# Kernel tuning notes

Measured on AMD Instinct MI355X. Metric: run time of the kernel, lower is better.

The kernel has to match this reference:

```python
import jax, jax.numpy as jnp
import numpy as np
import math

B, T, D, H = 4, 1024, 1024, 16
DK = D // H
EPS = 1e-12  # F.normalize eps

def setup_inputs() -> dict:
    key = jax.random.key(0)
    ks = jax.random.split(key, 6)
    xav = math.sqrt(6.0 / (D + D))  # xavier_uniform bound for square Linear
    x = jax.random.normal(ks[0], (B, T, D), dtype=jnp.float32)
    Wq = jax.random.uniform(ks[1], (D, D), jnp.float32, -xav, xav)
    Wk = jax.random.uniform(ks[2], (D, D), jnp.float32, -xav, xav)
    Wv = jax.random.uniform(ks[3], (D, D), jnp.float32, -xav, xav)
    Wo = jax.random.uniform(ks[4], (D, D), jnp.float32, -xav, xav)
    logit_g = math.log(0.9 / 0.1)
    logit_l = math.log(0.1 / 0.9)
    W_gamma = jnp.zeros((H,), jnp.float32)
    b_gamma = jnp.full((H,), logit_g, jnp.float32)
    W_lambda = jnp.zeros((H,), jnp.float32)
    b_lambda = jnp.full((H,), logit_l, jnp.float32)
    return {"x": x, "Wq": Wq, "Wk": Wk, "Wv": Wv, "Wo": Wo,
            "W_gamma": W_gamma, "b_gamma": b_gamma,
            "W_lambda": W_lambda, "b_lambda": b_lambda}

def reference(x, Wq, Wk, Wv, Wo, W_gamma, b_gamma, W_lambda, b_lambda):
    b, t, d = x.shape
    # projections (torch Linear: x @ W.T), split heads -> [T, B, H, dk] for scan
    def proj(W):
        return jnp.einsum('btd,ed->bte', x, W).reshape(b, t, H, DK).transpose(1, 0, 2, 3)
    q = proj(Wq)
    k = proj(Wk)
    v = proj(Wv)
    # L2-normalize k along dk (F.normalize semantics)
    k = k / jnp.maximum(jnp.linalg.norm(k, axis=-1, keepdims=True), EPS)
    k_bar = k.mean(axis=-1)  # [T, B, H]
    gamma = jax.nn.sigmoid(W_gamma * k_bar + b_gamma)
    lam = jax.nn.sigmoid(W_lambda * k_bar + b_lambda)
    rho = (1.0 - lam) * gamma  # [T, B, H]

    S0 = jnp.zeros((b, H, DK, DK), x.dtype)

    def step(S, inp):
        q_t, k_t, v_t, rho_t = inp  # [B,H,dk] x3, [B,H]
        r = rho_t[..., None, None]
        S = r * S + (1.0 - r) * jnp.einsum('bhv,bhk->bhvk', v_t, k_t)
        y_t = jnp.einsum('bhv,bhvk->bhk', q_t, S)
        return S, y_t

    _, ys = jax.lax.scan(step, S0, (q, k, v, rho))  # ys: [T, B, H, dk]
    out = ys.transpose(1, 0, 2, 3).reshape(b, t, d)
    return jnp.einsum('btd,ed->bte', out, Wo)
```

## Files before the change

### kernel.cpp

```cpp
#include <hip/hip_runtime.h>
#include <hip/hip_bf16.h>


typedef __bf16 b16x8 __attribute__((ext_vector_type(8)));
typedef float  f32x4 __attribute__((ext_vector_type(4)));
typedef unsigned short u16x8 __attribute__((ext_vector_type(8)));
using bf16_t = __hip_bfloat16;

#define AS1C(p) ((const __attribute__((address_space(1))) void*)(p))
#define AS3(p)  ((__attribute__((address_space(3))) void*)(p))

__device__ __forceinline__ void g2l16(const void* g, void* l) {
  __builtin_amdgcn_global_load_lds(AS1C(g), AS3(l), 16, 0, 0);
}
__device__ __forceinline__ void g2l4(const void* g, void* l) {
  __builtin_amdgcn_global_load_lds(AS1C(g), AS3(l), 4, 0, 0);
}

__device__ __forceinline__ unsigned short f2b(float x) {
  unsigned u = __float_as_uint(x);
  return (unsigned short)((u + 0x7FFFu + ((u >> 16) & 1u)) >> 16);
}
__device__ __forceinline__ float b2f(unsigned short b) {
  return __uint_as_float(((unsigned)b) << 16);
}

__device__ __forceinline__ int wire_flag(const unsigned* __restrict__ x, int tid) {
  unsigned u = x[tid & 63];
  int e = (int)((u >> 23) & 0xFF);
  unsigned long long m = __ballot(e >= 95 && e <= 135);
  return (__popcll(m) >= 32) ? 1 : 0;
}

__global__ __launch_bounds__(256)
void convert_all(const void* __restrict__ x,
                 const void* __restrict__ w0, const void* __restrict__ w1,
                 const void* __restrict__ w2, const void* __restrict__ w3,
                 unsigned short* __restrict__ xb,
                 unsigned short* __restrict__ wb0, unsigned short* __restrict__ wb1,
                 unsigned short* __restrict__ wb2, unsigned short* __restrict__ wb3)
{
  const int fm = wire_flag((const unsigned*)x, threadIdx.x);
  const long i8 = ((long)blockIdx.x * 256 + threadIdx.x) * 8;
  const void* src; unsigned short* dst; long off;
  if (i8 < 4194304) { src = x; dst = xb; off = i8; }
  else {
    long j = i8 - 4194304;
    int w = (int)(j >> 20); off = j & 1048575;
    src = (w == 0) ? w0 : (w == 1) ? w1 : (w == 2) ? w2 : w3;
    dst = (w == 0) ? wb0 : (w == 1) ? wb1 : (w == 2) ? wb2 : wb3;
  }
  if (fm) {
    const float4 a = *(const float4*)((const float*)src + off);
    const float4 b = *(const float4*)((const float*)src + off + 4);
    u16x8 o;
    o[0] = f2b(a.x); o[1] = f2b(a.y); o[2] = f2b(a.z); o[3] = f2b(a.w);
    o[4] = f2b(b.x); o[5] = f2b(b.y); o[6] = f2b(b.z); o[7] = f2b(b.w);
    *(u16x8*)(dst + off) = o;
  } else {
    *(int4*)(dst + off) = *(const int4*)((const unsigned short*)src + off);
  }
}

__global__ __launch_bounds__(256)
void gemm_qkv(const unsigned* __restrict__ xraw,
              const bf16_t* __restrict__ A,
              const bf16_t* __restrict__ B0, const bf16_t* __restrict__ B1,
              const bf16_t* __restrict__ B2,
              unsigned short* __restrict__ C0, unsigned short* __restrict__ C1,
              unsigned short* __restrict__ C2,
              const void* __restrict__ Wg, const void* __restrict__ bg,
              const void* __restrict__ Wl, const void* __restrict__ bl,
              float* __restrict__ rho)
{
  constexpr int K = 1024, N = 1024;
  const int flat = blockIdx.x;
  const int xcd = flat & 7, sl = flat >> 3;
  const int z = sl >> 5, t5 = sl & 31;
  const int bx = ((xcd & 1) << 2) | (t5 & 3);
  const int by = ((xcd >> 1) << 3) | (t5 >> 2);
  const bf16_t* B = (z == 0) ? B0 : (z == 1) ? B1 : B2;
  unsigned short* C = (z == 0) ? C0 : (z == 1) ? C1 : C2;
  __shared__ __align__(16) unsigned short As[128 * 32];
  __shared__ __align__(16) unsigned short Bs[128 * 32];
  const int tid  = threadIdx.x;
  const int lane = tid & 63;
  const int wave = tid >> 6;
  const int wm = wave >> 1, wn = wave & 1;
  const int quad = lane >> 4, tm = lane & 15;
  const long row0 = (long)by * 128;
  const long col0 = (long)bx * 128;

  f32x4 acc[4][4];
#pragma unroll
  for (int i = 0; i < 4; ++i)
#pragma unroll
    for (int j = 0; j < 4; ++j) acc[i][j] = (f32x4){0.f, 0.f, 0.f, 0.f};

  const int sr = tid >> 2;
  const int scc = tid & 3;
  const int qg = (scc - (sr >> 1)) & 3;
  const bf16_t* ap = A + (row0 + sr) * (long)K + qg * 8;
  const bf16_t* bp = B + (col0 + sr) * (long)K + qg * 8;
  unsigned short* la = As + tid * 8;
  unsigned short* lb = Bs + tid * 8;
  const int cc = (quad + ((tm >> 1) & 3)) & 3;

  for (int kt = 0; kt < K; kt += 32) {
    __syncthreads();
    g2l16(ap + kt,           la);
    g2l16(ap + 64l * K + kt, la + 2048);
    g2l16(bp + kt,           lb);
    g2l16(bp + 64l * K + kt, lb + 2048);
    __syncthreads();

    b16x8 af[4], bfr[4];
#pragma unroll
    for (int i = 0; i < 4; ++i)
      af[i] = *(const b16x8*)&As[(wm * 64 + i * 16 + tm) * 32 + cc * 8];
#pragma unroll
    for (int j = 0; j < 4; ++j)
      bfr[j] = *(const b16x8*)&Bs[(wn * 64 + j * 16 + tm) * 32 + cc * 8];
#pragma unroll
    for (int i = 0; i < 4; ++i)
#pragma unroll
      for (int j = 0; j < 4; ++j)
        acc[i][j] = __builtin_amdgcn_mfma_f32_16x16x32_bf16(af[i], bfr[j], acc[i][j], 0, 0, 0);
  }

  if (z != 1) {
#pragma unroll
    for (int i = 0; i < 4; ++i)
#pragma unroll
      for (int j = 0; j < 4; ++j)
#pragma unroll
        for (int r = 0; r < 4; ++r) {
          long row = row0 + wm * 64 + i * 16 + quad * 4 + r;
          long col = col0 + wn * 64 + j * 16 + tm;
          C[row * N + col] = f2b(acc[i][j][r]);
        }
  } else {
    const int fm = wire_flag(xraw, tid);
    const int h = bx * 2 + wn;
    float wgv, bgv, wlv, blv;
    if (fm) {
      wgv = ((const float*)Wg)[h]; bgv = ((const float*)bg)[h];
      wlv = ((const float*)Wl)[h]; blv = ((const float*)bl)[h];
    } else {
      wgv = b2f(((const unsigned short*)Wg)[h]); bgv = b2f(((const unsigned short*)bg)[h]);
      wlv = b2f(((const unsigned short*)Wl)[h]); blv = b2f(((const unsigned short*)bl)[h]);
    }
#pragma unroll
    for (int i = 0; i < 4; ++i)
#pragma unroll
      for (int r = 0; r < 4; ++r) {
        float ss = 0.f, sv = 0.f;
#pragma unroll
        for (int j = 0; j < 4; ++j) {
          const float v = acc[i][j][r];
          ss += v * v; sv += v;
        }
#pragma unroll
        for (int m = 1; m < 16; m <<= 1) {
          ss += __shfl_xor(ss, m);
          sv += __shfl_xor(sv, m);
        }
        const float inv = 1.f / fmaxf(sqrtf(ss), 1e-12f);
        const long row = row0 + wm * 64 + i * 16 + quad * 4 + r;
#pragma unroll
        for (int j = 0; j < 4; ++j)
          C[row * N + col0 + wn * 64 + j * 16 + tm] = f2b(acc[i][j][r] * inv);
        if (tm == 0) {
          const float kbar = sv * inv * (1.f / 64.f);
          const float gm = 1.f / (1.f + expf(-(wgv * kbar + bgv)));
          const float lm = 1.f / (1.f + expf(-(wlv * kbar + blv)));
          const int b = (int)(row >> 10), t = (int)(row & 1023);
          rho[(size_t)(b * 16 + h) * 1024 + t] = (1.f - lm) * gm;
        }
      }
  }
}

__global__ __launch_bounds__(256)
void gemm_out64(const unsigned* __restrict__ xraw,
                const bf16_t* __restrict__ A, const bf16_t* __restrict__ B,
                void* __restrict__ C)
{
  constexpr int K = 1024, N = 1024;
  const int flat = blockIdx.x;
  const int xcd = flat & 7, sl = flat >> 3;
  const int bx = sl & 15;
  const int by = (xcd << 3) | (sl >> 4);
  __shared__ __align__(16) unsigned short As[64 * 64];
  __shared__ __align__(16) unsigned short Bs[64 * 64];
  const int tid  = threadIdx.x;
  const int lane = tid & 63;
  const int wave = tid >> 6;
  const int quad = lane >> 4, tm = lane & 15;
  const long row0 = (long)by * 64;
  const long col0 = (long)bx * 64;

  f32x4 acc[4];
#pragma unroll
  for (int i = 0; i < 4; ++i) acc[i] = (f32x4){0.f, 0.f, 0.f, 0.f};

  const int sr = tid >> 2;
  const int scc = tid & 3;
  const int qg = (scc - (sr >> 1)) & 3;
  const bf16_t* ap = A + (row0 + sr) * (long)K + qg * 8;
  const bf16_t* bp = B + (col0 + sr) * (long)K + qg * 8;
  unsigned short* la = As + tid * 8;
  unsigned short* lb = Bs + tid * 8;
  const int cc = (quad + ((tm >> 1) & 3)) & 3;

  for (int kt = 0; kt < K; kt += 64) {
    __syncthreads();
    g2l16(ap + kt,      la);
    g2l16(ap + kt + 32, la + 2048);
    g2l16(bp + kt,      lb);
    g2l16(bp + kt + 32, lb + 2048);
    __syncthreads();

    b16x8 bf0 = *(const b16x8*)&Bs[(wave * 16 + tm) * 32 + cc * 8];
    b16x8 bf1 = *(const b16x8*)&Bs[2048 + (wave * 16 + tm) * 32 + cc * 8];
#pragma unroll
    for (int i = 0; i < 4; ++i) {
      b16x8 a0 = *(const b16x8*)&As[(i * 16 + tm) * 32 + cc * 8];
      b16x8 a1 = *(const b16x8*)&As[2048 + (i * 16 + tm) * 32 + cc * 8];
      acc[i] = __builtin_amdgcn_mfma_f32_16x16x32_bf16(a0, bf0, acc[i], 0, 0, 0);
      acc[i] = __builtin_amdgcn_mfma_f32_16x16x32_bf16(a1, bf1, acc[i], 0, 0, 0);
    }
  }

  const int fm = wire_flag(xraw, tid);
#pragma unroll
  for (int i = 0; i < 4; ++i)
#pragma unroll
    for (int r = 0; r < 4; ++r) {
      const long row = row0 + i * 16 + quad * 4 + r;
      const long col = col0 + wave * 16 + tm;
      const float v = acc[i][r];
      if (fm) ((float*)C)[row * N + col] = v;
      else    ((unsigned short*)C)[row * N + col] = f2b(v);
    }
}

__device__ __forceinline__ void stage_chunk_x(const unsigned short* G, int n0c, int h,
                                              unsigned short* lds, int tid) {
#pragma unroll
  for (int sh = 0; sh < 2; ++sh) {
    const int idx = sh * 256 + tid;
    const int row = idx >> 3, c2 = idx & 7;
    const int gc = c2 ^ (row & 7);
    g2l16(G + (size_t)(n0c + row) * 1024 + h * 64 + gc * 8, lds + idx * 8);
  }
}
__device__ __forceinline__ void stage_blk_x(const unsigned short* G,
                                            unsigned short* lds, int tid) {
#pragma unroll
  for (int sh = 0; sh < 2; ++sh) {
    const int idx = sh * 256 + tid;
    const int row = idx >> 3, c2 = idx & 7;
    const int gc = c2 ^ (row & 7);
    g2l16(G + row * 64 + gc * 8, lds + idx * 8);
  }
}
__device__ __forceinline__ b16x8 rdx(const unsigned short* lds, int row, int k0) {
  return *(const b16x8*)&lds[row * 64 + (((k0 >> 3) ^ (row & 7)) << 3)];
}
__device__ __forceinline__ float rdx1(const unsigned short* lds, int row, int col) {
  return b2f(lds[row * 64 + (((col >> 3) ^ (row & 7)) << 3) + (col & 7)]);
}

__device__ __forceinline__ void transpose_x(const unsigned short* src,
                                            unsigned short* dst,
                                            const float* sc, int tid) {
  const int kc = tid & 63;
  const int s4 = (tid >> 6) * 16;
  u16x8 o0, o1;
#pragma unroll
  for (int i = 0; i < 16; ++i) {
    const int s = s4 + i;
    float v = rdx1(src, s, kc);
    if (sc) v *= sc[s];
    const unsigned short b = f2b(v);
    if (i < 8) o0[i] = b; else o1[i - 8] = b;
  }
  *(u16x8*)&dst[kc * 72 + s4]     = o0;
  *(u16x8*)&dst[kc * 72 + s4 + 8] = o1;
}

__device__ __forceinline__ void rho_scan(const float* rho_s, float* aw, float* cw,
                                         float* sc, int tid) {
  if (tid < 64) {
    const float r = rho_s[tid];
    float p = r;
#pragma unroll
    for (int d = 1; d < 64; d <<= 1) {
      float o = __shfl_up(p, d);
      if (tid >= d) p *= o;
    }
    aw[tid] = p;
    const float c = (1.f - r) / p;
    cw[tid] = c;
    const float Ac = __shfl(p, 63);
    sc[tid] = Ac * c;
  }
}

__global__ __launch_bounds__(256)
void chunk_outer(const unsigned short* __restrict__ Kb, const unsigned short* __restrict__ Vb,
                 const float* __restrict__ rho, unsigned short* __restrict__ Ug,
                 float* __restrict__ A_g)
{
  __shared__ __align__(16) unsigned short ks[4096];
  __shared__ __align__(16) unsigned short vs[4096];
  __shared__ __align__(16) unsigned short kt[64 * 72];
  __shared__ __align__(16) unsigned short vt[64 * 72];
  __shared__ float rho_s[64], aw[64], cw[64], sc[64];
  const int tid = threadIdx.x;
  const int bid = blockIdx.x;
  const int bh = bid >> 4, c = bid & 15;
  const int b = bh >> 4, h = bh & 15;
  const int n0c = b * 1024 + c * 64;
  const int lane = tid & 63, wave = tid >> 6;
  const int quad = lane >> 4, tm = lane & 15;

  stage_chunk_x(Kb, n0c, h, ks, tid);
  stage_chunk_x(Vb, n0c, h, vs, tid);
  if (tid < 64) g2l4(rho + (size_t)bh * 1024 + c * 64 + tid, rho_s + tid);
  __syncthreads();
  rho_scan(rho_s, aw, cw, sc, tid);
  __syncthreads();
  transpose_x(ks, kt, sc, tid);
  transpose_x(vs, vt, nullptr, tid);
  __syncthreads();

  const int mrow = 16 * wave + tm;
  b16x8 a0 = *(const b16x8*)&kt[mrow * 72 + quad * 8];
  b16x8 a1 = *(const b16x8*)&kt[mrow * 72 + 32 + quad * 8];
#pragma unroll
  for (int j4 = 0; j4 < 4; ++j4) {
    const int nrow = 16 * j4 + tm;
    b16x8 b0 = *(const b16x8*)&vt[nrow * 72 + quad * 8];
    b16x8 b1 = *(const b16x8*)&vt[nrow * 72 + 32 + quad * 8];
    f32x4 acc = (f32x4){0.f, 0.f, 0.f, 0.f};
    acc = __builtin_amdgcn_mfma_f32_16x16x32_bf16(a0, b0, acc, 0, 0, 0);
    acc = __builtin_amdgcn_mfma_f32_16x16x32_bf16(a1, b1, acc, 0, 0, 0);
#pragma unroll
    for (int r = 0; r < 4; ++r) {
      const int kc = 16 * wave + quad * 4 + r;
      Ug[(size_t)bid * 4096 + kc * 64 + 16 * j4 + tm] = f2b(acc[r]);
    }
  }
  if (tid == 0) A_g[bid] = aw[63];
}

__global__ __launch_bounds__(256)
void chunk_scan(const unsigned short* __restrict__ Ug, const float* __restrict__ A_g,
                unsigned short* __restrict__ Sp)
{
  const int bh = blockIdx.x >> 4;
  const int e  = (blockIdx.x & 15) * 256 + threadIdx.x;
  const size_t base = (size_t)bh * 16 * 4096 + e;
  float S = 0.f;
#pragma unroll
  for (int c = 0; c < 16; ++c) {
    Sp[base + (size_t)c * 4096] = f2b(S);
    S = A_g[bh * 16 + c] * S + b2f(Ug[base + (size_t)c * 4096]);
  }
}

__global__ __launch_bounds__(256)
void chunk_y(const unsigned short* __restrict__ Qb, const unsigned short* __restrict__ Kb,
             const unsigned short* __restrict__ Vb, const unsigned short* __restrict__ Sp,
             const float* __restrict__ rho, unsigned short* __restrict__ Yb)
{
  __shared__ __align__(16) unsigned short qs[4096];
  __shared__ __align__(16) unsigned short ks[4096];
  __shared__ __align__(16) unsigned short vs[4096];
  __shared__ __align__(16) unsigned short ss[4096];
  __shared__ __align__(16) unsigned short kt[64 * 72];
  __shared__ __align__(16) unsigned short pt[64 * 72];
  __shared__ float rho_s[64], aw[64], cw[64], sc[64];
  const int tid = threadIdx.x;
  const int bid = blockIdx.x;
  const int bh = bid >> 4, c = bid & 15;
  const int b = bh >> 4, h = bh & 15;
  const int n0c = b * 1024 + c * 64;
  const int lane = tid & 63, wave = tid >> 6;
  const int quad = lane >> 4, tm = lane & 15;

  stage_chunk_x(Qb, n0c, h, qs, tid);
  stage_chunk_x(Kb, n0c, h, ks, tid);
  stage_chunk_x(Vb, n0c, h, vs, tid);
  stage_blk_x(Sp + (size_t)bid * 4096, ss, tid);
  if (tid < 64) g2l4(rho + (size_t)bh * 1024 + c * 64 + tid, rho_s + tid);
  __syncthreads();
  rho_scan(rho_s, aw, cw, sc, tid);
  __syncthreads();
  transpose_x(ks, kt, nullptr, tid);

  __bf16* ptb = (__bf16*)pt;
  const int trow = 16 * wave + tm;

  b16x8 af_q[2];
#pragma unroll
  for (int kk = 0; kk < 2; ++kk)
    af_q[kk] = rdx(qs, trow, kk * 32 + quad * 8);
#pragma unroll
  for (int j4 = 0; j4 < 4; ++j4) {
    f32x4 acc = (f32x4){0.f, 0.f, 0.f, 0.f};
#pragma unroll
    for (int kk = 0; kk < 2; ++kk) {
      const b16x8 bf = rdx(vs, 16 * j4 + tm, kk * 32 + quad * 8);
      acc = __builtin_amdgcn_mfma_f32_16x16x32_bf16(af_q[kk], bf, acc, 0, 0, 0);
    }
    const int s = 16 * j4 + tm;
    const float cws = cw[s];
#pragma unroll
    for (int r = 0; r < 4; ++r) {
      const int t = 16 * wave + quad * 4 + r;
      const float w = (s <= t) ? aw[t] * cws : 0.f;
      ptb[t * 72 + s] = (__bf16)(acc[r] * w);
    }
  }

  const float at = aw[trow];
  b16x8 af_qs[2], af_p[2];
#pragma unroll
  for (int kk = 0; kk < 2; ++kk) {
    b16x8 t8;
#pragma unroll
    for (int j = 0; j < 8; ++j) t8[j] = (__bf16)(at * (float)af_q[kk][j]);
    af_qs[kk] = t8;
    af_p[kk] = *(const b16x8*)&pt[trow * 72 + kk * 32 + quad * 8];
  }
  __syncthreads();

#pragma unroll
  for (int j4 = 0; j4 < 4; ++j4) {
    const int kc = 16 * j4 + tm;
    f32x4 acc = (f32x4){0.f, 0.f, 0.f, 0.f};
#pragma unroll
    for (int kk = 0; kk < 2; ++kk) {
      const int kbase = kk * 32 + quad * 8;
      const b16x8 bk = *(const b16x8*)&kt[kc * 72 + kbase];
      const b16x8 bs = rdx(ss, kc, kbase);
      acc = __builtin_amdgcn_mfma_f32_16x16x32_bf16(af_p[kk],  bk, acc, 0, 0, 0);
      acc = __builtin_amdgcn_mfma_f32_16x16x32_bf16(af_qs[kk], bs, acc, 0, 0, 0);
    }
#pragma unroll
    for (int r = 0; r < 4; ++r) {
      const int t = 16 * wave + quad * 4 + r;
      Yb[(size_t)(n0c + t) * 1024 + h * 64 + kc] = f2b(acc[r]);
    }
  }
}

extern "C" void kernel_launch(void* const* d_in, const int* in_sizes, int n_in,
                              void* d_out, int out_size, void* d_ws, size_t ws_size,
                              hipStream_t stream) {
  const void* x  = d_in[0];
  const void* Wq = d_in[1];
  const void* Wk = d_in[2];
  const void* Wv = d_in[3];
  const void* Wo = d_in[4];

  char* ws = (char*)d_ws;
  const size_t MB = 1ull << 20;
  unsigned short* x_b  = (unsigned short*)(ws);
  unsigned short* Wq_b = (unsigned short*)(ws + 8 * MB);
  unsigned short* Wk_b = (unsigned short*)(ws + 10 * MB);
  unsigned short* Wv_b = (unsigned short*)(ws + 12 * MB);
  unsigned short* Wo_b = (unsigned short*)(ws + 14 * MB);
  unsigned short* Qb = (unsigned short*)(ws + 16 * MB);
  unsigned short* Kb = (unsigned short*)(ws + 24 * MB);
  unsigned short* Vb = (unsigned short*)(ws + 32 * MB);
  unsigned short* Yb = (unsigned short*)(ws + 40 * MB);
  unsigned short* Ug = (unsigned short*)(ws + 48 * MB);
  unsigned short* Sp = (unsigned short*)(ws + 64 * MB);
  float*  rh   = (float*)(ws + 72 * MB);
  float*  A_g  = (float*)(ws + 72 * MB + 256 * 1024);

  dim3 blk(256);
  convert_all<<<dim3(4096), blk, 0, stream>>>(x, Wq, Wk, Wv, Wo,
                                              x_b, Wq_b, Wk_b, Wv_b, Wo_b);
  gemm_qkv<<<dim3(768), blk, 0, stream>>>((const unsigned*)x,
      (const bf16_t*)x_b, (const bf16_t*)Wq_b, (const bf16_t*)Wk_b, (const bf16_t*)Wv_b,
      Qb, Kb, Vb, d_in[5], d_in[6], d_in[7], d_in[8], rh);
  chunk_outer<<<dim3(1024), blk, 0, stream>>>(Kb, Vb, rh, Ug, A_g);
  chunk_scan<<<dim3(1024), blk, 0, stream>>>(Ug, A_g, Sp);
  chunk_y<<<dim3(1024), blk, 0, stream>>>(Qb, Kb, Vb, Sp, rh, Yb);
  gemm_out64<<<dim3(1024), blk, 0, stream>>>((const unsigned*)x,
      (const bf16_t*)Yb, (const bf16_t*)Wo_b, d_out);
}
```

Before: 168.9 us.

## Fuse chunked scan into one sequential per-head kernel and widen GEMM K tile

Replaces the three chunk kernels (outer products, inter-chunk scan, intra-chunk output) with one kernel per batch-head. It walks the 16 chunks sequentially, keeps the running state in registers and LDS, and double-buffers the Q/K/V chunk loads. This removes the global round trips for the per-chunk updates and prefix states, plus two launches. The cost is that the grid shrinks from 1024 to 64 blocks and the chunks are serialized. The QKV GEMM also moves to a 64-wide K tile with XOR-swizzled LDS, which halves the barriers per K step.

```diff
diff --git a/kernel.cpp b/kernel.cpp
--- a/kernel.cpp
+++ b/kernel.cpp
@@ -12,9 +12,6 @@
 
 __device__ __forceinline__ void g2l16(const void* g, void* l) {
   __builtin_amdgcn_global_load_lds(AS1C(g), AS3(l), 16, 0, 0);
-}
-__device__ __forceinline__ void g2l4(const void* g, void* l) {
-  __builtin_amdgcn_global_load_lds(AS1C(g), AS3(l), 4, 0, 0);
 }
 
 __device__ __forceinline__ unsigned short f2b(float x) {
@@ -81,8 +78,8 @@
   const int by = ((xcd >> 1) << 3) | (t5 >> 2);
   const bf16_t* B = (z == 0) ? B0 : (z == 1) ? B1 : B2;
   unsigned short* C = (z == 0) ? C0 : (z == 1) ? C1 : C2;
-  __shared__ __align__(16) unsigned short As[128 * 32];
-  __shared__ __align__(16) unsigned short Bs[128 * 32];
+  __shared__ __align__(16) unsigned short As[128 * 64];
+  __shared__ __align__(16) unsigned short Bs[128 * 64];
   const int tid  = threadIdx.x;
   const int lane = tid & 63;
   const int wave = tid >> 6;
@@ -97,35 +94,39 @@
 #pragma unroll
     for (int j = 0; j < 4; ++j) acc[i][j] = (f32x4){0.f, 0.f, 0.f, 0.f};
 
-  const int sr = tid >> 2;
-  const int scc = tid & 3;
-  const int qg = (scc - (sr >> 1)) & 3;
-  const bf16_t* ap = A + (row0 + sr) * (long)K + qg * 8;
-  const bf16_t* bp = B + (col0 + sr) * (long)K + qg * 8;
+  const int sr = tid >> 3;
+  const int c2 = tid & 7;
+  const int gc = c2 ^ (sr & 7);
+  const bf16_t* ap = A + (row0 + sr) * (long)K + gc * 8;
+  const bf16_t* bp = B + (col0 + sr) * (long)K + gc * 8;
   unsigned short* la = As + tid * 8;
   unsigned short* lb = Bs + tid * 8;
-  const int cc = (quad + ((tm >> 1) & 3)) & 3;
-
-  for (int kt = 0; kt < K; kt += 32) {
-    __syncthreads();
-    g2l16(ap + kt,           la);
-    g2l16(ap + 64l * K + kt, la + 2048);
-    g2l16(bp + kt,           lb);
-    g2l16(bp + 64l * K + kt, lb + 2048);
-    __syncthreads();
-
-    b16x8 af[4], bfr[4];
-#pragma unroll
-    for (int i = 0; i < 4; ++i)
-      af[i] = *(const b16x8*)&As[(wm * 64 + i * 16 + tm) * 32 + cc * 8];
-#pragma unroll
-    for (int j = 0; j < 4; ++j)
-      bfr[j] = *(const b16x8*)&Bs[(wn * 64 + j * 16 + tm) * 32 + cc * 8];
-#pragma unroll
-    for (int i = 0; i < 4; ++i)
+
+  for (int kt = 0; kt < K; kt += 64) {
+    __syncthreads();
+#pragma unroll
+    for (int sh = 0; sh < 4; ++sh) {
+      g2l16(ap + (long)sh * 32 * K + kt, la + sh * 2048);
+      g2l16(bp + (long)sh * 32 * K + kt, lb + sh * 2048);
+    }
+    __syncthreads();
+
+#pragma unroll
+    for (int kk = 0; kk < 2; ++kk) {
+      const int pcsel = ((kk * 4 + quad) ^ (tm & 7)) << 3;
+      b16x8 af[4], bfr[4];
+#pragma unroll
+      for (int i = 0; i < 4; ++i)
+        af[i] = *(const b16x8*)&As[(wm * 64 + i * 16 + tm) * 64 + pcsel];
 #pragma unroll
       for (int j = 0; j < 4; ++j)
-        acc[i][j] = __builtin_amdgcn_mfma_f32_16x16x32_bf16(af[i], bfr[j], acc[i][j], 0, 0, 0);
+        bfr[j] = *(const b16x8*)&Bs[(wn * 64 + j * 16 + tm) * 64 + pcsel];
+#pragma unroll
+      for (int i = 0; i < 4; ++i)
+#pragma unroll
+        for (int j = 0; j < 4; ++j)
+          acc[i][j] = __builtin_amdgcn_mfma_f32_16x16x32_bf16(af[i], bfr[j], acc[i][j], 0, 0, 0);
+    }
   }
 
   if (z != 1) {
@@ -255,16 +256,6 @@
     g2l16(G + (size_t)(n0c + row) * 1024 + h * 64 + gc * 8, lds + idx * 8);
   }
 }
-__device__ __forceinline__ void stage_blk_x(const unsigned short* G,
-                                            unsigned short* lds, int tid) {
-#pragma unroll
-  for (int sh = 0; sh < 2; ++sh) {
-    const int idx = sh * 256 + tid;
-    const int row = idx >> 3, c2 = idx & 7;
-    const int gc = c2 ^ (row & 7);
-    g2l16(G + row * 64 + gc * 8, lds + idx * 8);
-  }
-}
 __device__ __forceinline__ b16x8 rdx(const unsigned short* lds, int row, int k0) {
   return *(const b16x8*)&lds[row * 64 + (((k0 >> 3) ^ (row & 7)) << 3)];
 }
@@ -273,188 +264,156 @@
 }
 
 __device__ __forceinline__ void transpose_x(const unsigned short* src,
-                                            unsigned short* dst,
-                                            const float* sc, int tid) {
+                                            unsigned short* dst, int tid) {
   const int kc = tid & 63;
   const int s4 = (tid >> 6) * 16;
   u16x8 o0, o1;
 #pragma unroll
   for (int i = 0; i < 16; ++i) {
-    const int s = s4 + i;
-    float v = rdx1(src, s, kc);
-    if (sc) v *= sc[s];
-    const unsigned short b = f2b(v);
+    const unsigned short b = f2b(rdx1(src, s4 + i, kc));
     if (i < 8) o0[i] = b; else o1[i - 8] = b;
   }
   *(u16x8*)&dst[kc * 72 + s4]     = o0;
   *(u16x8*)&dst[kc * 72 + s4 + 8] = o1;
 }
 
-__device__ __forceinline__ void rho_scan(const float* rho_s, float* aw, float* cw,
-                                         float* sc, int tid) {
-  if (tid < 64) {
-    const float r = rho_s[tid];
-    float p = r;
-#pragma unroll
-    for (int d = 1; d < 64; d <<= 1) {
-      float o = __shfl_up(p, d);
-      if (tid >= d) p *= o;
-    }
-    aw[tid] = p;
-    const float c = (1.f - r) / p;
-    cw[tid] = c;
-    const float Ac = __shfl(p, 63);
-    sc[tid] = Ac * c;
-  }
-}
-
 __global__ __launch_bounds__(256)
-void chunk_outer(const unsigned short* __restrict__ Kb, const unsigned short* __restrict__ Vb,
-                 const float* __restrict__ rho, unsigned short* __restrict__ Ug,
-                 float* __restrict__ A_g)
+void chunk_all(const unsigned short* __restrict__ Qb, const unsigned short* __restrict__ Kb,
+               const unsigned short* __restrict__ Vb, const float* __restrict__ rho,
+               unsigned short* __restrict__ Yb)
 {
-  __shared__ __align__(16) unsigned short ks[4096];
-  __shared__ __align__(16) unsigned short vs[4096];
+  __shared__ __align__(16) unsigned short qs[2][4096];
+  __shared__ __align__(16) unsigned short ks2[2][4096];
+  __shared__ __align__(16) unsigned short vs2[2][4096];
   __shared__ __align__(16) unsigned short kt[64 * 72];
   __shared__ __align__(16) unsigned short vt[64 * 72];
-  __shared__ float rho_s[64], aw[64], cw[64], sc[64];
+  __shared__ __align__(16) unsigned short pt[64 * 72];
+  __shared__ __align__(16) unsigned short ssb[64 * 72];
+  __shared__ __align__(16) float rho_all[1024];
+  __shared__ float aw[64], cw[64], scs[64];
   const int tid = threadIdx.x;
-  const int bid = blockIdx.x;
-  const int bh = bid >> 4, c = bid & 15;
+  const int bh = blockIdx.x;
   const int b = bh >> 4, h = bh & 15;
-  const int n0c = b * 1024 + c * 64;
   const int lane = tid & 63, wave = tid >> 6;
   const int quad = lane >> 4, tm = lane & 15;
-
-  stage_chunk_x(Kb, n0c, h, ks, tid);
-  stage_chunk_x(Vb, n0c, h, vs, tid);
-  if (tid < 64) g2l4(rho + (size_t)bh * 1024 + c * 64 + tid, rho_s + tid);
-  __syncthreads();
-  rho_scan(rho_s, aw, cw, sc, tid);
-  __syncthreads();
-  transpose_x(ks, kt, sc, tid);
-  transpose_x(vs, vt, nullptr, tid);
-  __syncthreads();
-
-  const int mrow = 16 * wave + tm;
-  b16x8 a0 = *(const b16x8*)&kt[mrow * 72 + quad * 8];
-  b16x8 a1 = *(const b16x8*)&kt[mrow * 72 + 32 + quad * 8];
-#pragma unroll
-  for (int j4 = 0; j4 < 4; ++j4) {
-    const int nrow = 16 * j4 + tm;
-    b16x8 b0 = *(const b16x8*)&vt[nrow * 72 + quad * 8];
-    b16x8 b1 = *(const b16x8*)&vt[nrow * 72 + 32 + quad * 8];
-    f32x4 acc = (f32x4){0.f, 0.f, 0.f, 0.f};
-    acc = __builtin_amdgcn_mfma_f32_16x16x32_bf16(a0, b0, acc, 0, 0, 0);
-    acc = __builtin_amdgcn_mfma_f32_16x16x32_bf16(a1, b1, acc, 0, 0, 0);
-#pragma unroll
-    for (int r = 0; r < 4; ++r) {
-      const int kc = 16 * wave + quad * 4 + r;
-      Ug[(size_t)bid * 4096 + kc * 64 + 16 * j4 + tm] = f2b(acc[r]);
-    }
-  }
-  if (tid == 0) A_g[bid] = aw[63];
-}
-
-__global__ __launch_bounds__(256)
-void chunk_scan(const unsigned short* __restrict__ Ug, const float* __restrict__ A_g,
-                unsigned short* __restrict__ Sp)
-{
-  const int bh = blockIdx.x >> 4;
-  const int e  = (blockIdx.x & 15) * 256 + threadIdx.x;
-  const size_t base = (size_t)bh * 16 * 4096 + e;
-  float S = 0.f;
-#pragma unroll
+  const int trow = 16 * wave + tm;
+
+  stage_chunk_x(Qb, b * 1024, h, qs[0], tid);
+  stage_chunk_x(Kb, b * 1024, h, ks2[0], tid);
+  stage_chunk_x(Vb, b * 1024, h, vs2[0], tid);
+  g2l16(rho + (size_t)bh * 1024 + tid * 4, rho_all + tid * 4);
+  {
+    unsigned* z = (unsigned*)ssb;
+#pragma unroll
+    for (int i = 0; i < 9; ++i) z[i * 256 + tid] = 0u;
+  }
+  float Sreg[4][4];
+#pragma unroll
+  for (int j4 = 0; j4 < 4; ++j4)
+#pragma unroll
+    for (int r = 0; r < 4; ++r) Sreg[j4][r] = 0.f;
+
   for (int c = 0; c < 16; ++c) {
-    Sp[base + (size_t)c * 4096] = f2b(S);
-    S = A_g[bh * 16 + c] * S + b2f(Ug[base + (size_t)c * 4096]);
-  }
-}
-
-__global__ __launch_bounds__(256)
-void chunk_y(const unsigned short* __restrict__ Qb, const unsigned short* __restrict__ Kb,
-             const unsigned short* __restrict__ Vb, const unsigned short* __restrict__ Sp,
-             const float* __restrict__ rho, unsigned short* __restrict__ Yb)
-{
-  __shared__ __align__(16) unsigned short qs[4096];
-  __shared__ __align__(16) unsigned short ks[4096];
-  __shared__ __align__(16) unsigned short vs[4096];
-  __shared__ __align__(16) unsigned short ss[4096];
-  __shared__ __align__(16) unsigned short kt[64 * 72];
-  __shared__ __align__(16) unsigned short pt[64 * 72];
-  __shared__ float rho_s[64], aw[64], cw[64], sc[64];
-  const int tid = threadIdx.x;
-  const int bid = blockIdx.x;
-  const int bh = bid >> 4, c = bid & 15;
-  const int b = bh >> 4, h = bh & 15;
-  const int n0c = b * 1024 + c * 64;
-  const int lane = tid & 63, wave = tid >> 6;
-  const int quad = lane >> 4, tm = lane & 15;
-
-  stage_chunk_x(Qb, n0c, h, qs, tid);
-  stage_chunk_x(Kb, n0c, h, ks, tid);
-  stage_chunk_x(Vb, n0c, h, vs, tid);
-  stage_blk_x(Sp + (size_t)bid * 4096, ss, tid);
-  if (tid < 64) g2l4(rho + (size_t)bh * 1024 + c * 64 + tid, rho_s + tid);
-  __syncthreads();
-  rho_scan(rho_s, aw, cw, sc, tid);
-  __syncthreads();
-  transpose_x(ks, kt, nullptr, tid);
-
-  __bf16* ptb = (__bf16*)pt;
-  const int trow = 16 * wave + tm;
-
-  b16x8 af_q[2];
-#pragma unroll
-  for (int kk = 0; kk < 2; ++kk)
-    af_q[kk] = rdx(qs, trow, kk * 32 + quad * 8);
-#pragma unroll
-  for (int j4 = 0; j4 < 4; ++j4) {
-    f32x4 acc = (f32x4){0.f, 0.f, 0.f, 0.f};
+    const int cur = c & 1;
+    __syncthreads();
+    if (c < 15) {
+      const int n0n = b * 1024 + (c + 1) * 64;
+      stage_chunk_x(Qb, n0n, h, qs[cur ^ 1], tid);
+      stage_chunk_x(Kb, n0n, h, ks2[cur ^ 1], tid);
+      stage_chunk_x(Vb, n0n, h, vs2[cur ^ 1], tid);
+    }
+    if (tid < 64) {
+      const float r = rho_all[c * 64 + tid];
+      float p = r;
+#pragma unroll
+      for (int d = 1; d < 64; d <<= 1) {
+        float o = __shfl_up(p, d);
+        if (tid >= d) p *= o;
+      }
+      aw[tid] = p;
+      const float cv = (1.f - r) / p;
+      cw[tid] = cv;
+      scs[tid] = __shfl(p, 63) * cv;
+    }
+    transpose_x(ks2[cur], kt, tid);
+    transpose_x(vs2[cur], vt, tid);
+    __syncthreads();
+
+    b16x8 af_q[2];
+#pragma unroll
+    for (int kk = 0; kk < 2; ++kk)
+      af_q[kk] = rdx(qs[cur], trow, kk * 32 + quad * 8);
+#pragma unroll
+    for (int j4 = 0; j4 < 4; ++j4) {
+      f32x4 acc = (f32x4){0.f, 0.f, 0.f, 0.f};
+#pragma unroll
+      for (int kk = 0; kk < 2; ++kk) {
+        const b16x8 bf = rdx(vs2[cur], 16 * j4 + tm, kk * 32 + quad * 8);
+        acc = __builtin_amdgcn_mfma_f32_16x16x32_bf16(af_q[kk], bf, acc, 0, 0, 0);
+      }
+      const int s = 16 * j4 + tm;
+      const float cws = cw[s];
+#pragma unroll
+      for (int r = 0; r < 4; ++r) {
+        const int t = 16 * wave + quad * 4 + r;
+        const float w = (s <= t) ? aw[t] * cws : 0.f;
+        ((__bf16*)pt)[t * 72 + s] = (__bf16)(acc[r] * w);
+      }
+    }
+
+    const float at = aw[trow];
+    b16x8 af_qs[2], af_p[2], af_ks[2];
 #pragma unroll
     for (int kk = 0; kk < 2; ++kk) {
-      const b16x8 bf = rdx(vs, 16 * j4 + tm, kk * 32 + quad * 8);
-      acc = __builtin_amdgcn_mfma_f32_16x16x32_bf16(af_q[kk], bf, acc, 0, 0, 0);
-    }
-    const int s = 16 * j4 + tm;
-    const float cws = cw[s];
-#pragma unroll
-    for (int r = 0; r < 4; ++r) {
-      const int t = 16 * wave + quad * 4 + r;
-      const float w = (s <= t) ? aw[t] * cws : 0.f;
-      ptb[t * 72 + s] = (__bf16)(acc[r] * w);
-    }
-  }
-
-  const float at = aw[trow];
-  b16x8 af_qs[2], af_p[2];
-#pragma unroll
-  for (int kk = 0; kk < 2; ++kk) {
-    b16x8 t8;
-#pragma unroll
-    for (int j = 0; j < 8; ++j) t8[j] = (__bf16)(at * (float)af_q[kk][j]);
-    af_qs[kk] = t8;
-    af_p[kk] = *(const b16x8*)&pt[trow * 72 + kk * 32 + quad * 8];
-  }
-  __syncthreads();
-
-#pragma unroll
-  for (int j4 = 0; j4 < 4; ++j4) {
-    const int kc = 16 * j4 + tm;
-    f32x4 acc = (f32x4){0.f, 0.f, 0.f, 0.f};
-#pragma unroll
-    for (int kk = 0; kk < 2; ++kk) {
+      b16x8 t8;
+#pragma unroll
+      for (int j = 0; j < 8; ++j) t8[j] = (__bf16)(at * (float)af_q[kk][j]);
+      af_qs[kk] = t8;
+      af_p[kk] = *(const b16x8*)&pt[trow * 72 + kk * 32 + quad * 8];
       const int kbase = kk * 32 + quad * 8;
-      const b16x8 bk = *(const b16x8*)&kt[kc * 72 + kbase];
-      const b16x8 bs = rdx(ss, kc, kbase);
-      acc = __builtin_amdgcn_mfma_f32_16x16x32_bf16(af_p[kk],  bk, acc, 0, 0, 0);
-      acc = __builtin_amdgcn_mfma_f32_16x16x32_bf16(af_qs[kk], bs, acc, 0, 0, 0);
-    }
-#pragma unroll
-    for (int r = 0; r < 4; ++r) {
-      const int t = 16 * wave + quad * 4 + r;
-      Yb[(size_t)(n0c + t) * 1024 + h * 64 + kc] = f2b(acc[r]);
-    }
+      const b16x8 kraw = *(const b16x8*)&kt[trow * 72 + kbase];
+      b16x8 k8;
+#pragma unroll
+      for (int j = 0; j < 8; ++j) k8[j] = (__bf16)(scs[kbase + j] * (float)kraw[j]);
+      af_ks[kk] = k8;
+    }
+
+    const int n0c = b * 1024 + c * 64;
+    f32x4 Uacc[4];
+#pragma unroll
+    for (int j4 = 0; j4 < 4; ++j4) {
+      const int kc = 16 * j4 + tm;
+      f32x4 yacc = (f32x4){0.f, 0.f, 0.f, 0.f};
+      f32x4 uacc = (f32x4){0.f, 0.f, 0.f, 0.f};
+#pragma unroll
+      for (int kk = 0; kk < 2; ++kk) {
+        const int kbase = kk * 32 + quad * 8;
+        const b16x8 bk = *(const b16x8*)&kt[kc * 72 + kbase];
+        const b16x8 bs = *(const b16x8*)&ssb[kc * 72 + kbase];
+        const b16x8 bv = *(const b16x8*)&vt[kc * 72 + kbase];
+        yacc = __builtin_amdgcn_mfma_f32_16x16x32_bf16(af_p[kk],  bk, yacc, 0, 0, 0);
+        yacc = __builtin_amdgcn_mfma_f32_16x16x32_bf16(af_qs[kk], bs, yacc, 0, 0, 0);
+        uacc = __builtin_amdgcn_mfma_f32_16x16x32_bf16(af_ks[kk], bv, uacc, 0, 0, 0);
+      }
+      Uacc[j4] = uacc;
+#pragma unroll
+      for (int r = 0; r < 4; ++r) {
+        const int t = 16 * wave + quad * 4 + r;
+        Yb[(size_t)(n0c + t) * 1024 + h * 64 + kc] = f2b(yacc[r]);
+      }
+    }
+
+    __syncthreads();
+    const float Ac = aw[63];
+#pragma unroll
+    for (int j4 = 0; j4 < 4; ++j4)
+#pragma unroll
+      for (int r = 0; r < 4; ++r) {
+        const float sn = Ac * Sreg[j4][r] + Uacc[j4][r];
+        Sreg[j4][r] = sn;
+        const int kc = 16 * wave + quad * 4 + r;
+        ssb[kc * 72 + 16 * j4 + tm] = f2b(sn);
+      }
   }
 }
 
@@ -478,10 +437,7 @@
   unsigned short* Kb = (unsigned short*)(ws + 24 * MB);
   unsigned short* Vb = (unsigned short*)(ws + 32 * MB);
   unsigned short* Yb = (unsigned short*)(ws + 40 * MB);
-  unsigned short* Ug = (unsigned short*)(ws + 48 * MB);
-  unsigned short* Sp = (unsigned short*)(ws + 64 * MB);
   float*  rh   = (float*)(ws + 72 * MB);
-  float*  A_g  = (float*)(ws + 72 * MB + 256 * 1024);
 
   dim3 blk(256);
   convert_all<<<dim3(4096), blk, 0, stream>>>(x, Wq, Wk, Wv, Wo,
@@ -489,9 +445,7 @@
   gemm_qkv<<<dim3(768), blk, 0, stream>>>((const unsigned*)x,
       (const bf16_t*)x_b, (const bf16_t*)Wq_b, (const bf16_t*)Wk_b, (const bf16_t*)Wv_b,
       Qb, Kb, Vb, d_in[5], d_in[6], d_in[7], d_in[8], rh);
-  chunk_outer<<<dim3(1024), blk, 0, stream>>>(Kb, Vb, rh, Ug, A_g);
-  chunk_scan<<<dim3(1024), blk, 0, stream>>>(Ug, A_g, Sp);
-  chunk_y<<<dim3(1024), blk, 0, stream>>>(Qb, Kb, Vb, Sp, rh, Yb);
+  chunk_all<<<dim3(64), blk, 0, stream>>>(Qb, Kb, Vb, rh, Yb);
   gemm_out64<<<dim3(1024), blk, 0, stream>>>((const unsigned*)x,
       (const bf16_t*)Yb, (const bf16_t*)Wo_b, d_out);
 }
```

After: 190.1 us. 1.13x slower.
